# Optimization experiments

Hardware: AMD Instinct MI355X
Metric: run time of the kernel (lower is better)

## Reference

```python
import jax, jax.numpy as jnp
import numpy as np
from jax import lax

G, CPG, KS, N = 8, 8, 3, 9  # groups, channels per group, kernel size, ks*ks


def conv2d(x, w, b=None, pad=1):
    y = lax.conv_general_dilated(x, w, (1, 1), [(pad, pad), (pad, pad)],
                                 dimension_numbers=('NCHW', 'OIHW', 'NCHW'))
    if b is not None:
        y = y + b[None, :, None, None]
    return y


def deform_group(x, f, pw, pb, mw, mb, cw):
    # x: sampled feature (anchor slice), f: offset source (motion slice); both (b,c,h,w)
    b, c, h, w = x.shape
    offset = conv2d(f, pw, pb)                      # (b, 2N, h, w)
    m = jax.nn.sigmoid(conv2d(f, mw, mb))           # (b, N, h, w) modulation
    off = jnp.transpose(offset, (0, 2, 3, 1))       # (b, h, w, 2N): first N rows(x), last N cols(y)
    rng = jnp.arange(-1, 2, dtype=x.dtype)
    pn_x = jnp.repeat(rng, KS)                      # kernel row offset, n = kr*3 + kc
    pn_y = jnp.tile(rng, KS)                        # kernel col offset
    p0_x = jnp.arange(1, h + 1, dtype=x.dtype)[:, None, None]  # base grid starts at 1 (padding=0 here)
    p0_y = jnp.arange(1, w + 1, dtype=x.dtype)[None, :, None]
    px = p0_x + pn_x + off[..., :N]                 # (b, h, w, N)
    py = p0_y + pn_y + off[..., N:]
    fx = jnp.floor(lax.stop_gradient(px))           # p.detach().floor() in the original
    fy = jnp.floor(lax.stop_gradient(py))
    qx_lt = jnp.clip(fx, 0, h - 1)
    qx_rb = jnp.clip(fx + 1, 0, h - 1)
    qy_lt = jnp.clip(fy, 0, w - 1)
    qy_rb = jnp.clip(fy + 1, 0, w - 1)
    px = jnp.clip(px, 0, h - 1)
    py = jnp.clip(py, 0, w - 1)
    g_lt = (1 + (qx_lt - px)) * (1 + (qy_lt - py))
    g_rb = (1 - (qx_rb - px)) * (1 - (qy_rb - py))
    g_lb = (1 + (qx_lt - px)) * (1 - (qy_rb - py))
    g_rt = (1 - (qx_rb - px)) * (1 + (qy_lt - py))
    x_flat = x.reshape(b, c, h * w)

    def gather(ix, iy):
        idx = (ix * w + iy).astype(jnp.int32).reshape(b, 1, -1)  # (b,1,h*w*N)
        return jnp.take_along_axis(x_flat, idx, axis=2).reshape(b, c, h, w, N)

    x_off = (g_lt[:, None] * gather(qx_lt, qy_lt) + g_rb[:, None] * gather(qx_rb, qy_rb)
             + g_lb[:, None] * gather(qx_lt, qy_rb) + g_rt[:, None] * gather(qx_rb, qy_lt))
    x_off = x_off * jnp.transpose(m, (0, 2, 3, 1))[:, None]      # apply modulation mask
    # fused equivalent of reshape to (b,c,h*3,w*3) + conv(k=3, stride=3, no bias)
    return jnp.einsum('bchwn,ocn->bohw', x_off, cw.reshape(cw.shape[0], c, N))


def reference(o, anchor, pw, pb, mw, mb, cw, w1, b1, w2, b2):
    b, C, h, w = anchor.shape
    xg = anchor.reshape(b, G, CPG, h, w).transpose(1, 0, 2, 3, 4)  # (G,b,c,h,w)
    fg = o.reshape(b, G, CPG, h, w).transpose(1, 0, 2, 3, 4)
    tg = jax.vmap(deform_group)(xg, fg, pw, pb, mw, mb, cw)        # (G,b,c,h,w)
    target = tg.transpose(1, 0, 2, 3, 4).reshape(b, C, h, w)
    target_ = jnp.concatenate([target, anchor], axis=1)            # (b,128,h,w)
    return target + conv2d(conv2d(target_, w1, b1), w2, b2)


def setup_inputs() -> dict:
    key = jax.random.key(0)
    ks = jax.random.split(key, 11)
    B, C, H, W = 4, 64, 128, 128
    return {
        'o': jax.random.normal(ks[0], (B, C, H, W), jnp.float32),
        'anchor': jax.random.normal(ks[1], (B, C, H, W), jnp.float32),
        'pw': jax.random.normal(ks[2], (G, 2 * N, CPG, 3, 3), jnp.float32) * 0.05,
        'pb': jax.random.normal(ks[3], (G, 2 * N), jnp.float32) * 0.05,
        'mw': jax.random.normal(ks[4], (G, N, CPG, 3, 3), jnp.float32) * 0.05,
        'mb': jax.random.normal(ks[5], (G, N), jnp.float32) * 0.05,
        'cw': jax.random.normal(ks[6], (G, CPG, CPG, 3, 3), jnp.float32) * 0.05,
        'w1': jax.random.normal(ks[7], (64, 128, 3, 3), jnp.float32) * 0.05,
        'b1': jax.random.normal(ks[8], (64,), jnp.float32) * 0.05,
        'w2': jax.random.normal(ks[9], (64, 64, 3, 3), jnp.float32) * 0.05,
        'b2': jax.random.normal(ks[10], (64,), jnp.float32) * 0.05,
    }
```

## Files before the change

### kernel.cpp

```cpp
#include <hip/hip_runtime.h>


typedef __attribute__((ext_vector_type(8))) short short8;
typedef __attribute__((ext_vector_type(4))) float float4v;

#define MFMA_B16(a, b, c) __builtin_amdgcn_mfma_f32_16x16x32_bf16(a, b, c, 0, 0, 0)

__device__ __forceinline__ ushort f2bf(float f) {
    union { float f; unsigned u; } v; v.f = f;
    unsigned r = v.u + 0x7FFFu + ((v.u >> 16) & 1u);
    return (ushort)(r >> 16);
}
__device__ __forceinline__ float bf2f(ushort h) {
    union { unsigned u; float f; } v; v.u = ((unsigned)h) << 16;
    return v.f;
}

__global__ __launch_bounds__(256) void prep(
    const float* __restrict__ anchor,
    const float* __restrict__ w1, const float* __restrict__ w2,
    const float* __restrict__ pw, const float* __restrict__ pb,
    const float* __restrict__ mw, const float* __restrict__ mb,
    const float* __restrict__ cw,
    ushort* __restrict__ anc_nhwc,
    ushort* __restrict__ rw1, ushort* __restrict__ rw2,
    ushort* __restrict__ rpwh, ushort* __restrict__ rpwl,
    ushort* __restrict__ rcw)
{
    const int blk = blockIdx.x;
    if (blk < 256) {
        int pix = (blk & 63) * 256 + threadIdx.x;
        int b = blk >> 6;
        ushort tmp[64];
        #pragma unroll
        for (int ch = 0; ch < 64; ++ch)
            tmp[ch] = f2bf(anchor[(((size_t)(b * 64 + ch)) << 14) + pix]);
        ushort* dp = anc_nhwc + (((size_t)b) << 20) + (size_t)pix * 64;
        #pragma unroll
        for (int grp = 0; grp < 8; ++grp) {
            short8 v;
            #pragma unroll
            for (int j = 0; j < 8; ++j) v[j] = (short)tmp[grp * 8 + j];
            *(short8*)(dp + grp * 8) = v;
        }
        return;
    }
    int i = (blk - 256) * 256 + threadIdx.x;
    if (i < 73728) {
        int ic = i & 127, r = i >> 7, oc = r & 63, s = r >> 6;
        rw1[i] = f2bf(w1[(oc * 128 + ic) * 9 + s]);
    }
    if (i < 36864) {
        int ic = i & 63, r = i >> 6, oc = r & 63, s = r >> 6;
        rw2[i] = f2bf(w2[(oc * 64 + ic) * 9 + s]);
    }
    if (i < 24576) {
        int k = i % 96, r = i / 96, n = r & 31, g = r >> 5;
        float v = 0.f;
        if (k < 72) {
            int s = k >> 3, ic = k & 7;
            if (n < 18)      v = pw[((g * 18 + n) * 8 + ic) * 9 + s];
            else if (n < 27) v = mw[((g * 9 + (n - 18)) * 8 + ic) * 9 + s];
        } else if (k == 72) {
            if (n < 18)      v = pb[g * 18 + n];
            else if (n < 27) v = mb[g * 9 + (n - 18)];
        }
        ushort h = f2bf(v);
        rpwh[i] = h;
        rpwl[i] = f2bf(v - bf2f(h));
    }
    if (i < 12288) {
        int k = i % 96, r = i / 96, oc = r & 15, g = r >> 4;
        float v = 0.f;
        if (k < 72 && oc < 8) {
            int n = k >> 3, ic = k & 7;
            v = cw[((g * 8 + oc) * 8 + ic) * 9 + n];
        }
        rcw[i] = f2bf(v);
    }
}

__global__ __launch_bounds__(256, 3) void deform_mfma(
    const float* __restrict__ o, const ushort* __restrict__ anc,
    const ushort* __restrict__ rpwh, const ushort* __restrict__ rpwl,
    const ushort* __restrict__ rcw,
    ushort* __restrict__ xcatA, float* __restrict__ target)
{
    const int tile = blockIdx.x, g = blockIdx.y, b = blockIdx.z;
    const int ty0 = (tile >> 3) * 16, tx0 = (tile & 7) * 16;
    const int tid = threadIdx.x, lane = tid & 63, wave = tid >> 6;
    const int l15 = lane & 15, quad = lane >> 4;

    __shared__ __align__(16) ushort sU[26624];
    ushort* slabh = sU;
    ushort* slabl = sU + 2592;
    float*  sOff  = (float*)(sU + 8192);

    const size_t nbase = ((size_t)b) << 20;

    for (int idx = tid; idx < 8 * 324; idx += 256) {
        int ic = idx / 324; int pix = idx - ic * 324;
        int r = pix / 18, c = pix - r * 18;
        int gy = ty0 + r - 1, gx = tx0 + c - 1;
        float v = 0.f;
        if ((unsigned)gy < 128u && (unsigned)gx < 128u)
            v = o[(((size_t)(b * 64 + g * 8 + ic)) << 14) + (gy << 7) + gx];
        ushort h = f2bf(v);
        slabh[pix * 8 + ic] = h;
        slabl[pix * 8 + ic] = f2bf(v - bf2f(h));
    }
    __syncthreads();

    float4v offacc[4][2] = {};
    #pragma unroll
    for (int ks = 0; ks < 3; ++ks) {
        short8 Bh[2], Bl[2];
        #pragma unroll
        for (int nf = 0; nf < 2; ++nf) {
            int off = (g * 32 + nf * 16 + l15) * 96 + ks * 32 + quad * 8;
            Bh[nf] = *(const short8*)(rpwh + off);
            Bl[nf] = *(const short8*)(rpwl + off);
        }
        short8 Ah[4], Al[4];
        if (ks < 2) {
            int s = ks * 4 + quad, sy = s / 3, sx = s - sy * 3;
            #pragma unroll
            for (int py = 0; py < 4; ++py) {
                int row = wave * 4 + py;
                int sl = ((row + sy) * 18 + l15 + sx) * 8;
                Ah[py] = *(const short8*)(&slabh[sl]);
                Al[py] = *(const short8*)(&slabl[sl]);
            }
        } else {
            #pragma unroll
            for (int py = 0; py < 4; ++py) {
                short8 zh = {0, 0, 0, 0, 0, 0, 0, 0};
                short8 zl = {0, 0, 0, 0, 0, 0, 0, 0};
                if (quad == 0) {
                    int row = wave * 4 + py;
                    int sl = ((row + 2) * 18 + l15 + 2) * 8;
                    zh = *(const short8*)(&slabh[sl]);
                    zl = *(const short8*)(&slabl[sl]);
                } else if (quad == 1) {
                    zh[0] = (short)0x3F80;
                }
                Ah[py] = zh; Al[py] = zl;
            }
        }
        #pragma unroll
        for (int py = 0; py < 4; ++py)
            #pragma unroll
            for (int nf = 0; nf < 2; ++nf) {
                offacc[py][nf] = MFMA_B16(Ah[py], Bh[nf], offacc[py][nf]);
                offacc[py][nf] = MFMA_B16(Ah[py], Bl[nf], offacc[py][nf]);
                offacc[py][nf] = MFMA_B16(Al[py], Bh[nf], offacc[py][nf]);
            }
    }
    #pragma unroll
    for (int py = 0; py < 4; ++py) {
        int p0 = (wave * 4 + py) * 16 + quad * 4;
        #pragma unroll
        for (int nf = 0; nf < 2; ++nf)
            #pragma unroll
            for (int reg = 0; reg < 4; ++reg)
                sOff[(p0 + reg) * 33 + nf * 16 + l15] = offacc[py][nf][reg];
    }
    __syncthreads();

    const int p = tid;
    const int gy = ty0 + (p >> 4), gx = tx0 + (p & 15);
    float ox[9], oy[9], mz[9];
    #pragma unroll
    for (int n = 0; n < 9; ++n) {
        ox[n] = sOff[p * 33 + n];
        oy[n] = sOff[p * 33 + 9 + n];
        mz[n] = sOff[p * 33 + 18 + n];
    }
    __syncthreads();

    const ushort* ab = anc + nbase + g * 8;
    #pragma unroll
    for (int nb = 0; nb < 3; ++nb) {
        float Wlt[3], Wrb[3], Wlb[3], Wrt[3];
        short8 vlt[3], vrb[3], vlb[3], vrt[3];
        #pragma unroll
        for (int j = 0; j < 3; ++j) {
            const int n = nb * 3 + j;
            float pxf = (float)(gy + n / 3) + ox[n];
            float pyf = (float)(gx + n % 3) + oy[n];
            float fx = floorf(pxf), fy = floorf(pyf);
            float qxl = fminf(fmaxf(fx, 0.f), 127.f);
            float qxr = fminf(fmaxf(fx + 1.f, 0.f), 127.f);
            float qyl = fminf(fmaxf(fy, 0.f), 127.f);
            float qyr = fminf(fmaxf(fy + 1.f, 0.f), 127.f);
            float pxc = fminf(fmaxf(pxf, 0.f), 127.f);
            float pyc = fminf(fmaxf(pyf, 0.f), 127.f);
            float glx = 1.f + (qxl - pxc), grx = 1.f - (qxr - pxc);
            float gly = 1.f + (qyl - pyc), gry = 1.f - (qyr - pyc);
            float mm = 1.f / (1.f + __expf(-mz[n]));
            Wlt[j] = glx * gly * mm; Wrb[j] = grx * gry * mm;
            Wlb[j] = glx * gry * mm; Wrt[j] = grx * gly * mm;
            int ixl = (int)qxl, ixr = (int)qxr, iyl = (int)qyl, iyr = (int)qyr;
            vlt[j] = *(const short8*)(ab + (size_t)(ixl * 128 + iyl) * 64);
            vrb[j] = *(const short8*)(ab + (size_t)(ixr * 128 + iyr) * 64);
            vlb[j] = *(const short8*)(ab + (size_t)(ixl * 128 + iyr) * 64);
            vrt[j] = *(const short8*)(ab + (size_t)(ixr * 128 + iyl) * 64);
        }
        #pragma unroll
        for (int j = 0; j < 3; ++j) {
            const int n = nb * 3 + j;
            short8 sv;
            #pragma unroll
            for (int ic = 0; ic < 8; ++ic) {
                float val = Wlt[j] * bf2f((ushort)vlt[j][ic])
                          + Wrb[j] * bf2f((ushort)vrb[j][ic])
                          + Wlb[j] * bf2f((ushort)vlb[j][ic])
                          + Wrt[j] * bf2f((ushort)vrt[j][ic]);
                sv[ic] = (short)f2bf(val);
            }
            *(short8*)(&sU[p * 104 + n * 8]) = sv;
        }
    }
    {
        short8 z = {0, 0, 0, 0, 0, 0, 0, 0};
        *(short8*)(&sU[p * 104 + 72]) = z;
        *(short8*)(&sU[p * 104 + 80]) = z;
        *(short8*)(&sU[p * 104 + 88]) = z;
    }

    float4v cacc[4] = {};
    #pragma unroll
    for (int ks = 0; ks < 3; ++ks) {
        short8 Bw = *(const short8*)(rcw + ((g * 16 + l15) * 96 + ks * 32 + quad * 8));
        #pragma unroll
        for (int py = 0; py < 4; ++py) {
            int pp = (wave * 4 + py) * 16 + l15;
            short8 Af = *(const short8*)(&sU[pp * 104 + ks * 32 + quad * 8]);
            cacc[py] = MFMA_B16(Af, Bw, cacc[py]);
        }
    }
    #pragma unroll
    for (int py = 0; py < 4; ++py) {
        int pr = (wave * 4 + py) * 16 + quad * 4;
        if (l15 < 8) {
            #pragma unroll
            for (int reg = 0; reg < 4; ++reg)
                ((float*)&sU[(pr + reg) * 104])[l15] = cacc[py][reg];
        }
    }
    float res[8];
    #pragma unroll
    for (int oc = 0; oc < 8; ++oc) res[oc] = ((float*)&sU[p * 104])[oc];

    short8 pk;
    #pragma unroll
    for (int oc = 0; oc < 8; ++oc) pk[oc] = (short)f2bf(res[oc]);
    *(short8*)(xcatA + nbase + (size_t)(gy * 128 + gx) * 64 + g * 8) = pk;
    #pragma unroll
    for (int oc = 0; oc < 8; ++oc)
        target[(((size_t)(b * 64 + g * 8 + oc)) << 14) + gy * 128 + gx] = res[oc];
}

__global__ __launch_bounds__(256, 2) void conv1_mfma(
    const ushort* __restrict__ xA, const ushort* __restrict__ xB,
    const ushort* __restrict__ rw1, const float* __restrict__ b1,
    ushort* __restrict__ t1)
{
    const int patch = blockIdx.x, b = blockIdx.y;
    const int px0 = (patch & 7) * 16, py0 = (patch >> 3) * 8;
    const int tid = threadIdx.x, lane = tid & 63, wave = tid >> 6;
    const int mhalf = wave & 1, nhalf = wave >> 1;
    const int l15 = lane & 15, quad = lane >> 4;

    __shared__ __align__(16) ushort sA[180 * 136];

    short8 Bc[9][2];
    #pragma unroll
    for (int s = 0; s < 9; ++s)
        #pragma unroll
        for (int nf = 0; nf < 2; ++nf) {
            int oc = nhalf * 32 + nf * 16 + l15;
            Bc[s][nf] = *(const short8*)(rw1 + ((s * 64 + oc) * 128 + quad * 8));
        }

    const size_t nbase = ((size_t)b) << 20;
    for (int task = tid; task < 2880; task += 256) {
        int pix = task >> 4, grp = task & 15;
        int r = pix / 18, c = pix - r * 18;
        int gy = py0 + r - 1, gx = px0 + c - 1;
        short8 v = {0, 0, 0, 0, 0, 0, 0, 0};
        if ((unsigned)gy < 128u && (unsigned)gx < 128u) {
            const ushort* src = (grp < 8) ? xA : xB;
            v = *(const short8*)(src + nbase + (size_t)(gy * 128 + gx) * 64 + (grp & 7) * 8);
        }
        *(short8*)(&sA[pix * 136 + grp * 8]) = v;
    }
    __syncthreads();

    float4v acc[4][2] = {};
    #pragma unroll
    for (int ks = 0; ks < 4; ++ks) {
        short8 Bn[9][2];
        if (ks < 3) {
            #pragma unroll
            for (int s = 0; s < 9; ++s)
                #pragma unroll
                for (int nf = 0; nf < 2; ++nf) {
                    int oc = nhalf * 32 + nf * 16 + l15;
                    Bn[s][nf] = *(const short8*)(rw1 + ((s * 64 + oc) * 128 + (ks + 1) * 32 + quad * 8));
                }
        }
        #pragma unroll
        for (int r = 0; r < 6; ++r) {
            int slabrow = mhalf * 4 + r;
            short8 A[3];
            #pragma unroll
            for (int kx = 0; kx < 3; ++kx)
                A[kx] = *(const short8*)(&sA[(slabrow * 18 + l15 + kx) * 136 + ks * 32 + quad * 8]);
            #pragma unroll
            for (int ky = 0; ky < 3; ++ky) {
                int py = r - ky;
                if (py >= 0 && py < 4) {
                    #pragma unroll
                    for (int kx = 0; kx < 3; ++kx)
                        #pragma unroll
                        for (int nf = 0; nf < 2; ++nf)
                            acc[py][nf] = MFMA_B16(A[kx], Bc[ky * 3 + kx][nf], acc[py][nf]);
                }
            }
        }
        if (ks < 3) {
            #pragma unroll
            for (int s = 0; s < 9; ++s)
                #pragma unroll
                for (int nf = 0; nf < 2; ++nf) Bc[s][nf] = Bn[s][nf];
        }
    }
    #pragma unroll
    for (int nf = 0; nf < 2; ++nf) {
        int oc = nhalf * 32 + nf * 16 + l15;
        float bias = b1[oc];
        #pragma unroll
        for (int py = 0; py < 4; ++py) {
            int gy = py0 + mhalf * 4 + py;
            #pragma unroll
            for (int reg = 0; reg < 4; ++reg) {
                int gx = px0 + quad * 4 + reg;
                t1[nbase + (size_t)(gy * 128 + gx) * 64 + oc] = f2bf(acc[py][nf][reg] + bias);
            }
        }
    }
}

__global__ __launch_bounds__(256, 2) void conv2_mfma(
    const ushort* __restrict__ t1, const ushort* __restrict__ rw2,
    const float* __restrict__ b2, float* outres)
{
    const int patch = blockIdx.x, b = blockIdx.y;
    const int px0 = (patch & 7) * 16, py0 = (patch >> 3) * 8;
    const int tid = threadIdx.x, lane = tid & 63, wave = tid >> 6;
    const int ohalf = wave & 1, rhalf = wave >> 1;
    const int l15 = lane & 15, quad = lane >> 4;

    __shared__ __align__(16) ushort sX[180 * 72];

    short8 Ac[9][2];
    #pragma unroll
    for (int s = 0; s < 9; ++s)
        #pragma unroll
        for (int mf = 0; mf < 2; ++mf) {
            int oc = ohalf * 32 + mf * 16 + l15;
            Ac[s][mf] = *(const short8*)(rw2 + ((s * 64 + oc) * 64 + quad * 8));
        }

    const size_t nbase = ((size_t)b) << 20;
    for (int task = tid; task < 1440; task += 256) {
        int pix = task >> 3, grp = task & 7;
        int r = pix / 18, c = pix - r * 18;
        int gy = py0 + r - 1, gx = px0 + c - 1;
        short8 v = {0, 0, 0, 0, 0, 0, 0, 0};
        if ((unsigned)gy < 128u && (unsigned)gx < 128u)
            v = *(const short8*)(t1 + nbase + (size_t)(gy * 128 + gx) * 64 + grp * 8);
        *(short8*)(&sX[pix * 72 + grp * 8]) = v;
    }
    __syncthreads();

    float4v acc[2][4] = {};
    #pragma unroll
    for (int ks = 0; ks < 2; ++ks) {
        short8 An[9][2];
        if (ks < 1) {
            #pragma unroll
            for (int s = 0; s < 9; ++s)
                #pragma unroll
                for (int mf = 0; mf < 2; ++mf) {
                    int oc = ohalf * 32 + mf * 16 + l15;
                    An[s][mf] = *(const short8*)(rw2 + ((s * 64 + oc) * 64 + 32 + quad * 8));
                }
        }
        #pragma unroll
        for (int r = 0; r < 6; ++r) {
            int slabrow = rhalf * 4 + r;
            short8 Bx[3];
            #pragma unroll
            for (int kx = 0; kx < 3; ++kx)
                Bx[kx] = *(const short8*)(&sX[(slabrow * 18 + l15 + kx) * 72 + ks * 32 + quad * 8]);
            #pragma unroll
            for (int ky = 0; ky < 3; ++ky) {
                int py = r - ky;
                if (py >= 0 && py < 4) {
                    #pragma unroll
                    for (int kx = 0; kx < 3; ++kx)
                        #pragma unroll
                        for (int mf = 0; mf < 2; ++mf)
                            acc[mf][py] = MFMA_B16(Ac[ky * 3 + kx][mf], Bx[kx], acc[mf][py]);
                }
            }
        }
        if (ks < 1) {
            #pragma unroll
            for (int s = 0; s < 9; ++s)
                #pragma unroll
                for (int mf = 0; mf < 2; ++mf) Ac[s][mf] = An[s][mf];
        }
    }
    #pragma unroll
    for (int mf = 0; mf < 2; ++mf)
        #pragma unroll
        for (int reg = 0; reg < 4; ++reg) {
            int oc = ohalf * 32 + mf * 16 + quad * 4 + reg;
            float bias = b2[oc];
            #pragma unroll
            for (int py = 0; py < 4; ++py) {
                int gy = py0 + rhalf * 4 + py, gx = px0 + l15;
                size_t idx = (((size_t)(b * 64 + oc)) << 14) + gy * 128 + gx;
                outres[idx] = acc[mf][py][reg] + bias + outres[idx];
            }
        }
}

extern "C" void kernel_launch(void* const* d_in, const int* in_sizes, int n_in,
                              void* d_out, int out_size, void* d_ws, size_t ws_size,
                              hipStream_t stream) {
    const float* o      = (const float*)d_in[0];
    const float* anchor = (const float*)d_in[1];
    const float* pw     = (const float*)d_in[2];
    const float* pb     = (const float*)d_in[3];
    const float* mw     = (const float*)d_in[4];
    const float* mb     = (const float*)d_in[5];
    const float* cw     = (const float*)d_in[6];
    const float* w1     = (const float*)d_in[7];
    const float* b1     = (const float*)d_in[8];
    const float* w2     = (const float*)d_in[9];
    const float* b2     = (const float*)d_in[10];
    float* out = (float*)d_out;

    char* ws = (char*)d_ws;
    ushort* anc_nhwc = (ushort*)(ws);
    ushort* xcatA    = (ushort*)(ws + 8388608);
    ushort* t1b      = (ushort*)(ws + 16777216);
    char*   wsm      = ws + 25165824;
    ushort* rw1p     = (ushort*)(wsm);
    ushort* rw2p     = (ushort*)(wsm + 147456);
    ushort* rpwh     = (ushort*)(wsm + 147456 + 73728);
    ushort* rpwl     = (ushort*)(wsm + 147456 + 73728 + 49152);
    ushort* rcwp     = (ushort*)(wsm + 147456 + 73728 + 98304);

    prep<<<544, 256, 0, stream>>>(anchor, w1, w2, pw, pb, mw, mb, cw,
                                  anc_nhwc, rw1p, rw2p, rpwh, rpwl, rcwp);
    deform_mfma<<<dim3(64, 8, 4), 256, 0, stream>>>(o, anc_nhwc, rpwh, rpwl, rcwp,
                                                    xcatA, out );
    conv1_mfma<<<dim3(128, 4), 256, 0, stream>>>(xcatA, anc_nhwc, rw1p, b1, t1b);
    conv2_mfma<<<dim3(128, 4), 256, 0, stream>>>(t1b, rw2p, b2, out);
}
```

Before: 198.5 us.

## Use group-planar anchor/xcat layout and gather deform samples directly into MFMA fragments

Anchor and deform output buffers switch from NHWC (64 channels per pixel) to per-group planar layouts with 8 channels per pixel. Each group's bilinear gathers then hit a compact 2 MB plane instead of striding 128 bytes per pixel. The deform kernel computes the bilinear interpolation straight into MFMA A-fragments, with each quad handling taps n and n+4 and quad 0 handling tap 8. This removes the LDS staging of the 9x8 sampled columns, so shared memory shrinks and occupancy can rise from 3 to 4 blocks. conv1 loads are rewritten for the new layout, at the cost of less coalesced 16-byte loads across groups.

```diff
diff --git a/kernel.cpp b/kernel.cpp
--- a/kernel.cpp
+++ b/kernel.cpp
@@ -14,6 +14,42 @@
 __device__ __forceinline__ float bf2f(ushort h) {
     union { unsigned u; float f; } v; v.u = ((unsigned)h) << 16;
     return v.f;
+}
+
+__device__ __forceinline__ void tap_wo(int gy, int gx, int n,
+                                       float ox, float oy, float mzv,
+                                       float* W, int* O)
+{
+    int ky = n / 3, kx = n - ky * 3;
+    float pxf = (float)(gy + ky) + ox;
+    float pyf = (float)(gx + kx) + oy;
+    float fx = floorf(pxf), fy = floorf(pyf);
+    float qxl = fminf(fmaxf(fx, 0.f), 127.f);
+    float qxr = fminf(fmaxf(fx + 1.f, 0.f), 127.f);
+    float qyl = fminf(fmaxf(fy, 0.f), 127.f);
+    float qyr = fminf(fmaxf(fy + 1.f, 0.f), 127.f);
+    float pxc = fminf(fmaxf(pxf, 0.f), 127.f);
+    float pyc = fminf(fmaxf(pyf, 0.f), 127.f);
+    float glx = 1.f + (qxl - pxc), grx = 1.f - (qxr - pxc);
+    float gly = 1.f + (qyl - pyc), gry = 1.f - (qyr - pyc);
+    float mm = 1.f / (1.f + __expf(-mzv));
+    W[0] = glx * gly * mm; W[1] = grx * gry * mm;
+    W[2] = glx * gry * mm; W[3] = grx * gly * mm;
+    int ixl = (int)qxl, ixr = (int)qxr, iyl = (int)qyl, iyr = (int)qyr;
+    O[0] = ixl * 128 + iyl; O[1] = ixr * 128 + iyr;
+    O[2] = ixl * 128 + iyr; O[3] = ixr * 128 + iyl;
+}
+
+__device__ __forceinline__ short8 interp4(const float* W, const short8* cv)
+{
+    short8 out;
+    #pragma unroll
+    for (int ic = 0; ic < 8; ++ic) {
+        float v = W[0] * bf2f((ushort)cv[0][ic]) + W[1] * bf2f((ushort)cv[1][ic])
+                + W[2] * bf2f((ushort)cv[2][ic]) + W[3] * bf2f((ushort)cv[3][ic]);
+        out[ic] = (short)f2bf(v);
+    }
+    return out;
 }
 
 __global__ __launch_bounds__(256) void prep(
@@ -22,7 +58,7 @@
     const float* __restrict__ pw, const float* __restrict__ pb,
     const float* __restrict__ mw, const float* __restrict__ mb,
     const float* __restrict__ cw,
-    ushort* __restrict__ anc_nhwc,
+    ushort* __restrict__ anc_g,
     ushort* __restrict__ rw1, ushort* __restrict__ rw2,
     ushort* __restrict__ rpwh, ushort* __restrict__ rpwl,
     ushort* __restrict__ rcw)
@@ -35,13 +71,12 @@
         #pragma unroll
         for (int ch = 0; ch < 64; ++ch)
             tmp[ch] = f2bf(anchor[(((size_t)(b * 64 + ch)) << 14) + pix]);
-        ushort* dp = anc_nhwc + (((size_t)b) << 20) + (size_t)pix * 64;
         #pragma unroll
         for (int grp = 0; grp < 8; ++grp) {
             short8 v;
             #pragma unroll
             for (int j = 0; j < 8; ++j) v[j] = (short)tmp[grp * 8 + j];
-            *(short8*)(dp + grp * 8) = v;
+            *(short8*)(anc_g + ((size_t)(b * 8 + grp)) * 131072 + (size_t)pix * 8) = v;
         }
         return;
     }
@@ -80,23 +115,22 @@
     }
 }
 
-__global__ __launch_bounds__(256, 3) void deform_mfma(
-    const float* __restrict__ o, const ushort* __restrict__ anc,
+__global__ __launch_bounds__(256, 4) void deform_mfma(
+    const float* __restrict__ o, const ushort* __restrict__ anc_g,
     const ushort* __restrict__ rpwh, const ushort* __restrict__ rpwl,
     const ushort* __restrict__ rcw,
-    ushort* __restrict__ xcatA, float* __restrict__ target)
+    ushort* __restrict__ xcat_g, float* __restrict__ target)
 {
     const int tile = blockIdx.x, g = blockIdx.y, b = blockIdx.z;
     const int ty0 = (tile >> 3) * 16, tx0 = (tile & 7) * 16;
     const int tid = threadIdx.x, lane = tid & 63, wave = tid >> 6;
     const int l15 = lane & 15, quad = lane >> 4;
 
-    __shared__ __align__(16) ushort sU[26624];
+    __shared__ __align__(16) ushort sU[19008];
     ushort* slabh = sU;
     ushort* slabl = sU + 2592;
-    float*  sOff  = (float*)(sU + 8192);
-
-    const size_t nbase = ((size_t)b) << 20;
+    float*  sOff  = (float*)((char*)sU + 10368);
+    float*  sEp   = (float*)sU;
 
     for (int idx = tid; idx < 8 * 324; idx += 256) {
         int ic = idx / 324; int pix = idx - ic * 324;
@@ -160,109 +194,86 @@
     for (int py = 0; py < 4; ++py) {
         int p0 = (wave * 4 + py) * 16 + quad * 4;
         #pragma unroll
-        for (int nf = 0; nf < 2; ++nf)
+        for (int nf = 0; nf < 2; ++nf) {
+            int ch = nf * 16 + l15;
+            if (ch < 27) {
+                #pragma unroll
+                for (int reg = 0; reg < 4; ++reg)
+                    sOff[(p0 + reg) * 27 + ch] = offacc[py][nf][reg];
+            }
+        }
+    }
+
+    short8 Bw[3];
+    #pragma unroll
+    for (int ks = 0; ks < 3; ++ks)
+        Bw[ks] = *(const short8*)(rcw + ((g * 16 + l15) * 96 + ks * 32 + quad * 8));
+
+    const ushort* gb = anc_g + ((size_t)(b * 8 + g)) * 131072;
+    const int n1 = quad, n2 = quad + 4;
+    float4v cacc[4] = {};
+    #pragma unroll
+    for (int py = 0; py < 4; ++py) {
+        int prow = wave * 4 + py;
+        int p = prow * 16 + l15;
+        int gy = ty0 + prow, gx = tx0 + l15;
+
+        float W[8]; int O[8];
+        tap_wo(gy, gx, n1, sOff[p * 27 + n1], sOff[p * 27 + 9 + n1],
+               sOff[p * 27 + 18 + n1], &W[0], &O[0]);
+        tap_wo(gy, gx, n2, sOff[p * 27 + n2], sOff[p * 27 + 9 + n2],
+               sOff[p * 27 + 18 + n2], &W[4], &O[4]);
+        short8 cv[8];
+        #pragma unroll
+        for (int j = 0; j < 8; ++j)
+            cv[j] = *(const short8*)(gb + (size_t)O[j] * 8);
+        short8 A0 = interp4(&W[0], &cv[0]);
+        short8 A1 = interp4(&W[4], &cv[4]);
+        short8 A2 = {0, 0, 0, 0, 0, 0, 0, 0};
+        if (quad == 0) {
+            float W2[4]; int O2[4];
+            tap_wo(gy, gx, 8, sOff[p * 27 + 8], sOff[p * 27 + 17],
+                   sOff[p * 27 + 26], W2, O2);
+            short8 c2[4];
+            #pragma unroll
+            for (int j = 0; j < 4; ++j)
+                c2[j] = *(const short8*)(gb + (size_t)O2[j] * 8);
+            A2 = interp4(W2, c2);
+        }
+        cacc[py] = MFMA_B16(A0, Bw[0], cacc[py]);
+        cacc[py] = MFMA_B16(A1, Bw[1], cacc[py]);
+        cacc[py] = MFMA_B16(A2, Bw[2], cacc[py]);
+    }
+
+    __syncthreads();
+    #pragma unroll
+    for (int py = 0; py < 4; ++py) {
+        if (l15 < 8) {
             #pragma unroll
             for (int reg = 0; reg < 4; ++reg)
-                sOff[(p0 + reg) * 33 + nf * 16 + l15] = offacc[py][nf][reg];
+                sEp[((wave * 4 + py) * 16 + quad * 4 + reg) * 8 + l15] = cacc[py][reg];
+        }
     }
     __syncthreads();
-
-    const int p = tid;
-    const int gy = ty0 + (p >> 4), gx = tx0 + (p & 15);
-    float ox[9], oy[9], mz[9];
-    #pragma unroll
-    for (int n = 0; n < 9; ++n) {
-        ox[n] = sOff[p * 33 + n];
-        oy[n] = sOff[p * 33 + 9 + n];
-        mz[n] = sOff[p * 33 + 18 + n];
-    }
-    __syncthreads();
-
-    const ushort* ab = anc + nbase + g * 8;
-    #pragma unroll
-    for (int nb = 0; nb < 3; ++nb) {
-        float Wlt[3], Wrb[3], Wlb[3], Wrt[3];
-        short8 vlt[3], vrb[3], vlb[3], vrt[3];
-        #pragma unroll
-        for (int j = 0; j < 3; ++j) {
-            const int n = nb * 3 + j;
-            float pxf = (float)(gy + n / 3) + ox[n];
-            float pyf = (float)(gx + n % 3) + oy[n];
-            float fx = floorf(pxf), fy = floorf(pyf);
-            float qxl = fminf(fmaxf(fx, 0.f), 127.f);
-            float qxr = fminf(fmaxf(fx + 1.f, 0.f), 127.f);
-            float qyl = fminf(fmaxf(fy, 0.f), 127.f);
-            float qyr = fminf(fmaxf(fy + 1.f, 0.f), 127.f);
-            float pxc = fminf(fmaxf(pxf, 0.f), 127.f);
-            float pyc = fminf(fmaxf(pyf, 0.f), 127.f);
-            float glx = 1.f + (qxl - pxc), grx = 1.f - (qxr - pxc);
-            float gly = 1.f + (qyl - pyc), gry = 1.f - (qyr - pyc);
-            float mm = 1.f / (1.f + __expf(-mz[n]));
-            Wlt[j] = glx * gly * mm; Wrb[j] = grx * gry * mm;
-            Wlb[j] = glx * gry * mm; Wrt[j] = grx * gly * mm;
-            int ixl = (int)qxl, ixr = (int)qxr, iyl = (int)qyl, iyr = (int)qyr;
-            vlt[j] = *(const short8*)(ab + (size_t)(ixl * 128 + iyl) * 64);
-            vrb[j] = *(const short8*)(ab + (size_t)(ixr * 128 + iyr) * 64);
-            vlb[j] = *(const short8*)(ab + (size_t)(ixl * 128 + iyr) * 64);
-            vrt[j] = *(const short8*)(ab + (size_t)(ixr * 128 + iyl) * 64);
-        }
-        #pragma unroll
-        for (int j = 0; j < 3; ++j) {
-            const int n = nb * 3 + j;
-            short8 sv;
-            #pragma unroll
-            for (int ic = 0; ic < 8; ++ic) {
-                float val = Wlt[j] * bf2f((ushort)vlt[j][ic])
-                          + Wrb[j] * bf2f((ushort)vrb[j][ic])
-                          + Wlb[j] * bf2f((ushort)vlb[j][ic])
-                          + Wrt[j] * bf2f((ushort)vrt[j][ic]);
-                sv[ic] = (short)f2bf(val);
-            }
-            *(short8*)(&sU[p * 104 + n * 8]) = sv;
-        }
-    }
     {
-        short8 z = {0, 0, 0, 0, 0, 0, 0, 0};
-        *(short8*)(&sU[p * 104 + 72]) = z;
-        *(short8*)(&sU[p * 104 + 80]) = z;
-        *(short8*)(&sU[p * 104 + 88]) = z;
-    }
-
-    float4v cacc[4] = {};
-    #pragma unroll
-    for (int ks = 0; ks < 3; ++ks) {
-        short8 Bw = *(const short8*)(rcw + ((g * 16 + l15) * 96 + ks * 32 + quad * 8));
-        #pragma unroll
-        for (int py = 0; py < 4; ++py) {
-            int pp = (wave * 4 + py) * 16 + l15;
-            short8 Af = *(const short8*)(&sU[pp * 104 + ks * 32 + quad * 8]);
-            cacc[py] = MFMA_B16(Af, Bw, cacc[py]);
-        }
-    }
-    #pragma unroll
-    for (int py = 0; py < 4; ++py) {
-        int pr = (wave * 4 + py) * 16 + quad * 4;
-        if (l15 < 8) {
-            #pragma unroll
-            for (int reg = 0; reg < 4; ++reg)
-                ((float*)&sU[(pr + reg) * 104])[l15] = cacc[py][reg];
-        }
-    }
-    float res[8];
-    #pragma unroll
-    for (int oc = 0; oc < 8; ++oc) res[oc] = ((float*)&sU[p * 104])[oc];
-
-    short8 pk;
-    #pragma unroll
-    for (int oc = 0; oc < 8; ++oc) pk[oc] = (short)f2bf(res[oc]);
-    *(short8*)(xcatA + nbase + (size_t)(gy * 128 + gx) * 64 + g * 8) = pk;
-    #pragma unroll
-    for (int oc = 0; oc < 8; ++oc)
-        target[(((size_t)(b * 64 + g * 8 + oc)) << 14) + gy * 128 + gx] = res[oc];
+        const int p = tid;
+        const int gy = ty0 + (p >> 4), gx = tx0 + (p & 15);
+        float res[8];
+        #pragma unroll
+        for (int oc = 0; oc < 8; ++oc) res[oc] = sEp[p * 8 + oc];
+        short8 pk;
+        #pragma unroll
+        for (int oc = 0; oc < 8; ++oc) pk[oc] = (short)f2bf(res[oc]);
+        *(short8*)(xcat_g + ((size_t)(b * 8 + g)) * 131072
+                   + (size_t)((gy << 7) + gx) * 8) = pk;
+        #pragma unroll
+        for (int oc = 0; oc < 8; ++oc)
+            target[(((size_t)(b * 64 + g * 8 + oc)) << 14) + (gy << 7) + gx] = res[oc];
+    }
 }
 
 __global__ __launch_bounds__(256, 2) void conv1_mfma(
-    const ushort* __restrict__ xA, const ushort* __restrict__ xB,
+    const ushort* __restrict__ xg, const ushort* __restrict__ ag,
     const ushort* __restrict__ rw1, const float* __restrict__ b1,
     ushort* __restrict__ t1)
 {
@@ -283,15 +294,15 @@
             Bc[s][nf] = *(const short8*)(rw1 + ((s * 64 + oc) * 128 + quad * 8));
         }
 
-    const size_t nbase = ((size_t)b) << 20;
     for (int task = tid; task < 2880; task += 256) {
-        int pix = task >> 4, grp = task & 15;
+        int grp = task / 180, pix = task - grp * 180;
         int r = pix / 18, c = pix - r * 18;
         int gy = py0 + r - 1, gx = px0 + c - 1;
         short8 v = {0, 0, 0, 0, 0, 0, 0, 0};
         if ((unsigned)gy < 128u && (unsigned)gx < 128u) {
-            const ushort* src = (grp < 8) ? xA : xB;
-            v = *(const short8*)(src + nbase + (size_t)(gy * 128 + gx) * 64 + (grp & 7) * 8);
+            const ushort* plane = ((grp < 8) ? xg : ag)
+                                  + ((size_t)(b * 8 + (grp & 7))) * 131072;
+            v = *(const short8*)(plane + (size_t)((gy << 7) + gx) * 8);
         }
         *(short8*)(&sA[pix * 136 + grp * 8]) = v;
     }
@@ -336,6 +347,7 @@
                 for (int nf = 0; nf < 2; ++nf) Bc[s][nf] = Bn[s][nf];
         }
     }
+    const size_t nbase = ((size_t)b) << 20;
     #pragma unroll
     for (int nf = 0; nf < 2; ++nf) {
         int oc = nhalf * 32 + nf * 16 + l15;
@@ -456,20 +468,20 @@
     float* out = (float*)d_out;
 
     char* ws = (char*)d_ws;
-    ushort* anc_nhwc = (ushort*)(ws);
-    ushort* xcatA    = (ushort*)(ws + 8388608);
-    ushort* t1b      = (ushort*)(ws + 16777216);
-    char*   wsm      = ws + 25165824;
-    ushort* rw1p     = (ushort*)(wsm);
-    ushort* rw2p     = (ushort*)(wsm + 147456);
-    ushort* rpwh     = (ushort*)(wsm + 147456 + 73728);
-    ushort* rpwl     = (ushort*)(wsm + 147456 + 73728 + 49152);
-    ushort* rcwp     = (ushort*)(wsm + 147456 + 73728 + 98304);
+    ushort* anc_g  = (ushort*)(ws);
+    ushort* xcat_g = (ushort*)(ws + 8388608);
+    ushort* t1b    = (ushort*)(ws + 16777216);
+    char*   wsm    = ws + 25165824;
+    ushort* rw1p   = (ushort*)(wsm);
+    ushort* rw2p   = (ushort*)(wsm + 147456);
+    ushort* rpwh   = (ushort*)(wsm + 147456 + 73728);
+    ushort* rpwl   = (ushort*)(wsm + 147456 + 73728 + 49152);
+    ushort* rcwp   = (ushort*)(wsm + 147456 + 73728 + 98304);
 
     prep<<<544, 256, 0, stream>>>(anchor, w1, w2, pw, pb, mw, mb, cw,
-                                  anc_nhwc, rw1p, rw2p, rpwh, rpwl, rcwp);
-    deform_mfma<<<dim3(64, 8, 4), 256, 0, stream>>>(o, anc_nhwc, rpwh, rpwl, rcwp,
-                                                    xcatA, out );
-    conv1_mfma<<<dim3(128, 4), 256, 0, stream>>>(xcatA, anc_nhwc, rw1p, b1, t1b);
+                                  anc_g, rw1p, rw2p, rpwh, rpwl, rcwp);
+    deform_mfma<<<dim3(64, 8, 4), 256, 0, stream>>>(o, anc_g, rpwh, rpwl, rcwp,
+                                                    xcat_g, out );
+    conv1_mfma<<<dim3(128, 4), 256, 0, stream>>>(xcat_g, anc_g, rw1p, b1, t1b);
     conv2_mfma<<<dim3(128, 4), 256, 0, stream>>>(t1b, rw2p, b2, out);
 }
```

Measured after the change: 181.4 us. -8.6%, faster.
